# Optimization experiments

Measured on AMD Instinct MI355X. Metric: run time of the kernel, lower is better.

Reference implementation:

```python
import jax, jax.numpy as jnp
import numpy as np

N_NODES = 20000
N_EDGES = 320000
IN_CH = 256
HID_CH = 256   # 2 * out_channels
OUT_CH = 128


def gcn_conv(x, edge_index, W, b, n_nodes):
    """PyG GCNConv: linear transform, add self-loops, sym-normalized scatter-add."""
    x = x @ W  # [N, C_out]
    loop = jnp.arange(n_nodes, dtype=edge_index.dtype)
    row = jnp.concatenate([edge_index[0], loop])  # source nodes
    col = jnp.concatenate([edge_index[1], loop])  # destination nodes
    deg = jax.ops.segment_sum(jnp.ones_like(col, dtype=x.dtype), col,
                              num_segments=n_nodes)
    deg_inv_sqrt = jnp.where(deg > 0, jax.lax.rsqrt(deg), 0.0)
    norm = deg_inv_sqrt[row] * deg_inv_sqrt[col]  # [E+N]
    msg = x[row] * norm[:, None]                  # gather + scale
    out = jax.ops.segment_sum(msg, col, num_segments=n_nodes)  # scatter-add
    return out + b


def setup_inputs() -> dict:
    key = jax.random.key(0)
    k1, k2, k3, k4, k5 = jax.random.split(key, 5)
    doc_embeds = jax.random.normal(k1, (N_NODES, IN_CH), dtype=jnp.float32)
    edge_index = jax.random.randint(k2, (2, N_EDGES), 0, N_NODES, dtype=jnp.int64)
    # Glorot-style init for GCN weights, zero bias (PyG defaults)
    s1 = 1.0 / np.sqrt(IN_CH)
    s2 = 1.0 / np.sqrt(HID_CH)
    W1 = jax.random.uniform(k3, (IN_CH, HID_CH), jnp.float32, -s1, s1)
    b1 = jnp.zeros((HID_CH,), jnp.float32)
    W2 = jax.random.uniform(k4, (HID_CH, OUT_CH), jnp.float32, -s2, s2)
    b2 = jnp.zeros((OUT_CH,), jnp.float32)
    return {"doc_embeds": doc_embeds, "edge_index": edge_index,
            "W1": W1, "b1": b1, "W2": W2, "b2": b2}


def reference(doc_embeds, edge_index, W1, b1, W2, b2):
    n = doc_embeds.shape[0]
    x = jax.nn.relu(gcn_conv(doc_embeds, edge_index, W1, b1, n))
    x = gcn_conv(x, edge_index, W2, b2, n)
    return x
```

## Files before the change

kernel.cpp:

```cpp
#include <hip/hip_runtime.h>
#include <math.h>

#define N_NODES 20000
#define N_EDGES 320000
#define IN_CH   256
#define HID_CH  256
#define OUT_CH  128
#define CAP     64
#define GK      256

typedef __attribute__((ext_vector_type(8))) short short8;
typedef __attribute__((ext_vector_type(8))) unsigned short ushort8;
typedef __attribute__((ext_vector_type(4))) unsigned short ushort4v;
typedef __attribute__((ext_vector_type(2))) unsigned short ushort2v;
typedef __attribute__((ext_vector_type(4))) float floatx4;
typedef __attribute__((ext_vector_type(2))) float floatx2;
typedef __attribute__((ext_vector_type(2))) _Float16 half2v;

static __device__ __forceinline__ unsigned short f2bf(float f) {
    unsigned int u = __float_as_uint(f);
    u += 0x7FFFu + ((u >> 16) & 1u);
    return (unsigned short)(u >> 16);
}
static __device__ __forceinline__ float bf2f(unsigned short h) {
    return __uint_as_float(((unsigned int)h) << 16);
}

__global__ __launch_bounds__(256)
void prep_kernel(const float* __restrict__ W1, const float* __restrict__ W2,
                 const float* __restrict__ doc,
                 unsigned short* __restrict__ W1thi, unsigned short* __restrict__ W1tlo,
                 unsigned short* __restrict__ W2thi, unsigned short* __restrict__ W2tlo,
                 unsigned short* __restrict__ Ehi, unsigned short* __restrict__ Elo,
                 const int* __restrict__ row, const int* __restrict__ col,
                 int* __restrict__ deg, unsigned short* __restrict__ srcs) {
    const int g = blockIdx.x * blockDim.x + threadIdx.x;
    const int gsz = gridDim.x * blockDim.x;
    for (int t = g; t < (IN_CH * HID_CH) / 16; t += gsz) {
        int n = t >> 4;
        int kc = (t & 15) * 16;
        ushort8 h0, l0, h1, l1;
#pragma unroll
        for (int j = 0; j < 8; ++j) {
            float x = W1[(size_t)(kc + j) * HID_CH + n];
            h0[j] = f2bf(x); l0[j] = f2bf(x - bf2f(h0[j]));
            float y = W1[(size_t)(kc + 8 + j) * HID_CH + n];
            h1[j] = f2bf(y); l1[j] = f2bf(y - bf2f(h1[j]));
        }
        *(ushort8*)(W1thi + (size_t)n * IN_CH + kc)     = h0;
        *(ushort8*)(W1thi + (size_t)n * IN_CH + kc + 8) = h1;
        *(ushort8*)(W1tlo + (size_t)n * IN_CH + kc)     = l0;
        *(ushort8*)(W1tlo + (size_t)n * IN_CH + kc + 8) = l1;
    }
    for (int t = g; t < (HID_CH * OUT_CH) / 16; t += gsz) {
        int n = t >> 4;
        int kc = (t & 15) * 16;
        ushort8 h0, l0, h1, l1;
#pragma unroll
        for (int j = 0; j < 8; ++j) {
            float x = W2[(size_t)(kc + j) * OUT_CH + n];
            h0[j] = f2bf(x); l0[j] = f2bf(x - bf2f(h0[j]));
            float y = W2[(size_t)(kc + 8 + j) * OUT_CH + n];
            h1[j] = f2bf(y); l1[j] = f2bf(y - bf2f(h1[j]));
        }
        *(ushort8*)(W2thi + (size_t)n * HID_CH + kc)     = h0;
        *(ushort8*)(W2thi + (size_t)n * HID_CH + kc + 8) = h1;
        *(ushort8*)(W2tlo + (size_t)n * HID_CH + kc)     = l0;
        *(ushort8*)(W2tlo + (size_t)n * HID_CH + kc + 8) = l1;
    }
    for (int t = g; t < (N_NODES * IN_CH) / 16; t += gsz) {
        int node = t >> 4;
        int kc = (t & 15) * 16;
        const float* ap = doc + (size_t)node * IN_CH + kc;
        float4 f0 = *(const float4*)(ap);
        float4 f1 = *(const float4*)(ap + 4);
        float4 f2 = *(const float4*)(ap + 8);
        float4 f3 = *(const float4*)(ap + 12);
        float xs[16] = {f0.x, f0.y, f0.z, f0.w, f1.x, f1.y, f1.z, f1.w,
                        f2.x, f2.y, f2.z, f2.w, f3.x, f3.y, f3.z, f3.w};
        ushort8 h0, l0, h1, l1;
#pragma unroll
        for (int j = 0; j < 8; ++j) {
            h0[j] = f2bf(xs[j]);     l0[j] = f2bf(xs[j] - bf2f(h0[j]));
            h1[j] = f2bf(xs[8 + j]); l1[j] = f2bf(xs[8 + j] - bf2f(h1[j]));
        }
        *(ushort8*)(Ehi + (size_t)node * IN_CH + kc)     = h0;
        *(ushort8*)(Ehi + (size_t)node * IN_CH + kc + 8) = h1;
        *(ushort8*)(Elo + (size_t)node * IN_CH + kc)     = l0;
        *(ushort8*)(Elo + (size_t)node * IN_CH + kc + 8) = l1;
    }
    for (int i = g; i < N_EDGES; i += gsz) {
        int c = col[i];
        int r = row[i];
        int p = atomicAdd(&deg[c], 1);
        srcs[(size_t)c * CAP + p] = (unsigned short)r;
    }
}

template <int TN>
__global__ __launch_bounds__(256)
void gemm_mfma_kernel(const unsigned short* __restrict__ Ahi, const unsigned short* __restrict__ Alo,
                      const unsigned short* __restrict__ Bthi, const unsigned short* __restrict__ Btlo,
                      const int* __restrict__ deg, _Float16* __restrict__ C, int M, int N) {
    constexpr int NJ = TN / 32;
    __shared__ unsigned short As[2][64][36];
    __shared__ unsigned short Bs[2][TN][36];
    const int tid = threadIdx.x;
    const int m0 = blockIdx.y * 64;
    const int n0 = blockIdx.x * TN;
    const int lane = tid & 63;
    const int wave = tid >> 6;
    const int wr = (wave >> 1) * 32;
    const int wc = (wave & 1) * (TN / 2);
    const int lm = lane & 15;
    const int lk = (lane >> 4) * 8;

    floatx4 acc[2][NJ];
#pragma unroll
    for (int i = 0; i < 2; ++i)
#pragma unroll
        for (int j = 0; j < NJ; ++j) acc[i][j] = (floatx4){0.f, 0.f, 0.f, 0.f};

    const int ar  = tid >> 2;
    const int ako = (tid & 3) * 8;

    for (int k0 = 0; k0 < GK; k0 += 32) {
        {
            ushort8 vh = {}, vl = {};
            if (m0 + ar < M) {
                size_t ga = (size_t)(m0 + ar) * GK + k0 + ako;
                vh = *(const ushort8*)(Ahi + ga);
                vl = *(const ushort8*)(Alo + ga);
            }
            *(ushort8*)&As[0][ar][ako] = vh;
            *(ushort8*)&As[1][ar][ako] = vl;
        }
#pragma unroll
        for (int c = 0; c < TN / 64; ++c) {
            int ch = tid + c * 256;
            int r  = ch >> 2;
            int ko = (ch & 3) * 8;
            size_t gb = (size_t)(n0 + r) * GK + k0 + ko;
            *(ushort8*)&Bs[0][r][ko] = *(const ushort8*)(Bthi + gb);
            *(ushort8*)&Bs[1][r][ko] = *(const ushort8*)(Btlo + gb);
        }
        __syncthreads();

        short8 ah[2], al[2], bh[NJ], bl[NJ];
#pragma unroll
        for (int i = 0; i < 2; ++i) {
            ah[i] = *(const short8*)&As[0][wr + i * 16 + lm][lk];
            al[i] = *(const short8*)&As[1][wr + i * 16 + lm][lk];
        }
#pragma unroll
        for (int j = 0; j < NJ; ++j) {
            bh[j] = *(const short8*)&Bs[0][wc + j * 16 + lm][lk];
            bl[j] = *(const short8*)&Bs[1][wc + j * 16 + lm][lk];
        }
#pragma unroll
        for (int i = 0; i < 2; ++i)
#pragma unroll
            for (int j = 0; j < NJ; ++j) {
                acc[i][j] = __builtin_amdgcn_mfma_f32_16x16x32_bf16(ah[i], bh[j], acc[i][j], 0, 0, 0);
                acc[i][j] = __builtin_amdgcn_mfma_f32_16x16x32_bf16(ah[i], bl[j], acc[i][j], 0, 0, 0);
                acc[i][j] = __builtin_amdgcn_mfma_f32_16x16x32_bf16(al[i], bh[j], acc[i][j], 0, 0, 0);
            }
        __syncthreads();
    }

#pragma unroll
    for (int i = 0; i < 2; ++i) {
#pragma unroll
        for (int r = 0; r < 4; ++r) {
            int rowi = m0 + wr + i * 16 + (lane >> 4) * 4 + r;
            if (rowi < M) {
                float dr = 1.0f / sqrtf((float)(deg[rowi] + 1));
#pragma unroll
                for (int j = 0; j < NJ; ++j) {
                    C[(size_t)rowi * N + n0 + wc + j * 16 + lm] = (_Float16)(dr * acc[i][j][r]);
                }
            }
        }
    }
}

template <int C, int NSLICE, int MODE>
__global__ __launch_bounds__(256)
void gather_sliced_kernel(const _Float16* __restrict__ X, const int* __restrict__ deg,
                          const unsigned short* __restrict__ srcs,
                          const float* __restrict__ bias, float* __restrict__ outf,
                          unsigned short* __restrict__ outhi, unsigned short* __restrict__ outlo,
                          int n) {
    constexpr int SW = C / NSLICE;
    static_assert(SW == 32, "slice must be 32 channels");
    const int slice = blockIdx.x % NSLICE;
    const int ngrp  = blockIdx.x / NSLICE;
    const int wave = threadIdx.x >> 6;
    const int lane = threadIdx.x & 63;
    const int g  = lane >> 4;
    const int sl = lane & 15;
    const int node = ngrp * 16 + wave * 4 + g;
    if (node >= n) return;
    const int choff = slice * SW + sl * 2;
    const size_t beg = (size_t)node * CAP;
    const int cnt = deg[node];

    float a0 = 0.f, a1 = 0.f;
    int e = 0;
    for (; e + 4 <= cnt; e += 4) {
        ushort4v s4 = *(const ushort4v*)(srcs + beg + e);
        half2v v0 = *(const half2v*)(X + (size_t)s4.x * C + choff);
        half2v v1 = *(const half2v*)(X + (size_t)s4.y * C + choff);
        half2v v2 = *(const half2v*)(X + (size_t)s4.z * C + choff);
        half2v v3 = *(const half2v*)(X + (size_t)s4.w * C + choff);
        a0 += (float)v0.x + (float)v1.x + (float)v2.x + (float)v3.x;
        a1 += (float)v0.y + (float)v1.y + (float)v2.y + (float)v3.y;
    }
    for (; e < cnt; ++e) {
        int r = srcs[beg + e];
        half2v v = *(const half2v*)(X + (size_t)r * C + choff);
        a0 += (float)v.x; a1 += (float)v.y;
    }

    const float dc = 1.0f / sqrtf((float)(cnt + 1));
    half2v vsh = *(const half2v*)(X + (size_t)node * C + choff);
    float2 bb = *(const float2*)(bias + choff);

    float o0 = dc * (a0 + (float)vsh.x) + bb.x;
    float o1 = dc * (a1 + (float)vsh.y) + bb.y;

    if constexpr (MODE == 1) {
        float r0 = fmaxf(o0, 0.f), r1 = fmaxf(o1, 0.f);
        ushort2v hv, lv;
        hv.x = f2bf(r0); lv.x = f2bf(r0 - bf2f(hv.x));
        hv.y = f2bf(r1); lv.y = f2bf(r1 - bf2f(hv.y));
        *(ushort2v*)(outhi + (size_t)node * C + choff) = hv;
        *(ushort2v*)(outlo + (size_t)node * C + choff) = lv;
    } else {
        floatx2 o = {o0, o1};
        __builtin_nontemporal_store(o, (floatx2*)(outf + (size_t)node * C + choff));
    }
}

extern "C" void kernel_launch(void* const* d_in, const int* in_sizes, int n_in,
                              void* d_out, int out_size, void* d_ws, size_t ws_size,
                              hipStream_t stream) {
    const float* doc_embeds = (const float*)d_in[0];
    const int*   edge_index = (const int*)d_in[1];
    const float* W1 = (const float*)d_in[2];
    const float* b1 = (const float*)d_in[3];
    const float* W2 = (const float*)d_in[4];
    const float* b2 = (const float*)d_in[5];
    float* out = (float*)d_out;

    const int* row = edge_index;
    const int* col = edge_index + N_EDGES;

    char* ws = (char*)d_ws;
    auto au = [](size_t x) { return (x + 255) / 256 * 256; };

    _Float16* X1s = (_Float16*)ws;      ws += au((size_t)N_NODES * HID_CH * 2);
    unsigned short* Ehi  = (unsigned short*)ws; ws += au((size_t)N_NODES * IN_CH * 2);
    unsigned short* Elo  = (unsigned short*)ws; ws += au((size_t)N_NODES * IN_CH * 2);
    unsigned short* H1hi = (unsigned short*)ws; ws += au((size_t)N_NODES * HID_CH * 2);
    unsigned short* H1lo = (unsigned short*)ws; ws += au((size_t)N_NODES * HID_CH * 2);
    unsigned short* W1thi = (unsigned short*)ws; ws += au((size_t)IN_CH * HID_CH * 2);
    unsigned short* W1tlo = (unsigned short*)ws; ws += au((size_t)IN_CH * HID_CH * 2);
    unsigned short* W2thi = (unsigned short*)ws; ws += au((size_t)HID_CH * OUT_CH * 2);
    unsigned short* W2tlo = (unsigned short*)ws; ws += au((size_t)HID_CH * OUT_CH * 2);
    int*            deg   = (int*)ws;            ws += au((size_t)N_NODES * 4);
    unsigned short* srcs  = (unsigned short*)ws;

    hipMemsetAsync(deg, 0, (size_t)N_NODES * 4, stream);
    prep_kernel<<<(N_EDGES + 255) / 256, 256, 0, stream>>>(
        W1, W2, doc_embeds, W1thi, W1tlo, W2thi, W2tlo, Ehi, Elo, row, col, deg, srcs);

    {
        dim3 grid(HID_CH / 128, (N_NODES + 63) / 64);
        gemm_mfma_kernel<128><<<grid, 256, 0, stream>>>(
            Ehi, Elo, W1thi, W1tlo, deg, X1s, N_NODES, HID_CH);
    }
    gather_sliced_kernel<HID_CH, 8, 1><<<((N_NODES + 15) / 16) * 8, 256, 0, stream>>>(
        X1s, deg, srcs, b1, nullptr, H1hi, H1lo, N_NODES);

    {
        dim3 grid(OUT_CH / 64, (N_NODES + 63) / 64);
        gemm_mfma_kernel<64><<<grid, 256, 0, stream>>>(
            H1hi, H1lo, W2thi, W2tlo, deg, X1s, N_NODES, OUT_CH);
    }
    gather_sliced_kernel<OUT_CH, 4, 0><<<((N_NODES + 15) / 16) * 4, 256, 0, stream>>>(
        X1s, deg, srcs, b2, out, nullptr, nullptr, N_NODES);
}
```

Before: 181.9 us.

## Fuse fp32 split-bf16 conversion into GEMM1 and widen tiles and gather slices

The separate pass that split doc_embeds into hi/lo bf16 buffers is removed. GEMM1 now reads fp32 directly and does the split while staging to shared memory, which saves a full write and re-read of two 20000x256 bf16 arrays. Both GEMMs now cover the full N width in one block, so A is loaded once, and they declare a launch-bounds occupancy hint. The MFMA loop is reordered to load B fragments one at a time, and the gather kernels use 64-channel slices with 32 lanes per node. The trade-off is a larger accumulator per thread and therefore register pressure, plus fewer blocks in the GEMM grid.

Measured after the change: 176.3 us. 1.03x faster.

```diff
diff --git a/kernel.cpp b/kernel.cpp
--- a/kernel.cpp
+++ b/kernel.cpp
@@ -28,10 +28,8 @@
 
 __global__ __launch_bounds__(256)
 void prep_kernel(const float* __restrict__ W1, const float* __restrict__ W2,
-                 const float* __restrict__ doc,
                  unsigned short* __restrict__ W1thi, unsigned short* __restrict__ W1tlo,
                  unsigned short* __restrict__ W2thi, unsigned short* __restrict__ W2tlo,
-                 unsigned short* __restrict__ Ehi, unsigned short* __restrict__ Elo,
                  const int* __restrict__ row, const int* __restrict__ col,
                  int* __restrict__ deg, unsigned short* __restrict__ srcs) {
     const int g = blockIdx.x * blockDim.x + threadIdx.x;
@@ -68,27 +66,6 @@
         *(ushort8*)(W2tlo + (size_t)n * HID_CH + kc)     = l0;
         *(ushort8*)(W2tlo + (size_t)n * HID_CH + kc + 8) = l1;
     }
-    for (int t = g; t < (N_NODES * IN_CH) / 16; t += gsz) {
-        int node = t >> 4;
-        int kc = (t & 15) * 16;
-        const float* ap = doc + (size_t)node * IN_CH + kc;
-        float4 f0 = *(const float4*)(ap);
-        float4 f1 = *(const float4*)(ap + 4);
-        float4 f2 = *(const float4*)(ap + 8);
-        float4 f3 = *(const float4*)(ap + 12);
-        float xs[16] = {f0.x, f0.y, f0.z, f0.w, f1.x, f1.y, f1.z, f1.w,
-                        f2.x, f2.y, f2.z, f2.w, f3.x, f3.y, f3.z, f3.w};
-        ushort8 h0, l0, h1, l1;
-#pragma unroll
-        for (int j = 0; j < 8; ++j) {
-            h0[j] = f2bf(xs[j]);     l0[j] = f2bf(xs[j] - bf2f(h0[j]));
-            h1[j] = f2bf(xs[8 + j]); l1[j] = f2bf(xs[8 + j] - bf2f(h1[j]));
-        }
-        *(ushort8*)(Ehi + (size_t)node * IN_CH + kc)     = h0;
-        *(ushort8*)(Ehi + (size_t)node * IN_CH + kc + 8) = h1;
-        *(ushort8*)(Elo + (size_t)node * IN_CH + kc)     = l0;
-        *(ushort8*)(Elo + (size_t)node * IN_CH + kc + 8) = l1;
-    }
     for (int i = g; i < N_EDGES; i += gsz) {
         int c = col[i];
         int r = row[i];
@@ -97,9 +74,10 @@
     }
 }
 
-template <int TN>
-__global__ __launch_bounds__(256)
-void gemm_mfma_kernel(const unsigned short* __restrict__ Ahi, const unsigned short* __restrict__ Alo,
+template <int AMODE, int TN>
+__global__ __launch_bounds__(256, 2)
+void gemm_mfma_kernel(const float* __restrict__ Afp,
+                      const unsigned short* __restrict__ Ahi, const unsigned short* __restrict__ Alo,
                       const unsigned short* __restrict__ Bthi, const unsigned short* __restrict__ Btlo,
                       const int* __restrict__ deg, _Float16* __restrict__ C, int M, int N) {
     constexpr int NJ = TN / 32;
@@ -107,7 +85,6 @@
     __shared__ unsigned short Bs[2][TN][36];
     const int tid = threadIdx.x;
     const int m0 = blockIdx.y * 64;
-    const int n0 = blockIdx.x * TN;
     const int lane = tid & 63;
     const int wave = tid >> 6;
     const int wr = (wave >> 1) * 32;
@@ -128,9 +105,21 @@
         {
             ushort8 vh = {}, vl = {};
             if (m0 + ar < M) {
-                size_t ga = (size_t)(m0 + ar) * GK + k0 + ako;
-                vh = *(const ushort8*)(Ahi + ga);
-                vl = *(const ushort8*)(Alo + ga);
+                if (AMODE == 1) {
+                    const float* ap = Afp + (size_t)(m0 + ar) * GK + k0 + ako;
+                    float4 f0 = *(const float4*)ap;
+                    float4 f1 = *(const float4*)(ap + 4);
+                    float xs[8] = {f0.x, f0.y, f0.z, f0.w, f1.x, f1.y, f1.z, f1.w};
+#pragma unroll
+                    for (int j = 0; j < 8; ++j) {
+                        vh[j] = f2bf(xs[j]);
+                        vl[j] = f2bf(xs[j] - bf2f(vh[j]));
+                    }
+                } else {
+                    size_t ga = (size_t)(m0 + ar) * GK + k0 + ako;
+                    vh = *(const ushort8*)(Ahi + ga);
+                    vl = *(const ushort8*)(Alo + ga);
+                }
             }
             *(ushort8*)&As[0][ar][ako] = vh;
             *(ushort8*)&As[1][ar][ako] = vl;
@@ -140,13 +129,13 @@
             int ch = tid + c * 256;
             int r  = ch >> 2;
             int ko = (ch & 3) * 8;
-            size_t gb = (size_t)(n0 + r) * GK + k0 + ko;
+            size_t gb = (size_t)r * GK + k0 + ko;
             *(ushort8*)&Bs[0][r][ko] = *(const ushort8*)(Bthi + gb);
             *(ushort8*)&Bs[1][r][ko] = *(const ushort8*)(Btlo + gb);
         }
         __syncthreads();
 
-        short8 ah[2], al[2], bh[NJ], bl[NJ];
+        short8 ah[2], al[2];
 #pragma unroll
         for (int i = 0; i < 2; ++i) {
             ah[i] = *(const short8*)&As[0][wr + i * 16 + lm][lk];
@@ -154,17 +143,15 @@
         }
 #pragma unroll
         for (int j = 0; j < NJ; ++j) {
-            bh[j] = *(const short8*)&Bs[0][wc + j * 16 + lm][lk];
-            bl[j] = *(const short8*)&Bs[1][wc + j * 16 + lm][lk];
-        }
-#pragma unroll
-        for (int i = 0; i < 2; ++i)
-#pragma unroll
-            for (int j = 0; j < NJ; ++j) {
-                acc[i][j] = __builtin_amdgcn_mfma_f32_16x16x32_bf16(ah[i], bh[j], acc[i][j], 0, 0, 0);
-                acc[i][j] = __builtin_amdgcn_mfma_f32_16x16x32_bf16(ah[i], bl[j], acc[i][j], 0, 0, 0);
-                acc[i][j] = __builtin_amdgcn_mfma_f32_16x16x32_bf16(al[i], bh[j], acc[i][j], 0, 0, 0);
+            short8 bh = *(const short8*)&Bs[0][wc + j * 16 + lm][lk];
+            short8 bl = *(const short8*)&Bs[1][wc + j * 16 + lm][lk];
+#pragma unroll
+            for (int i = 0; i < 2; ++i) {
+                acc[i][j] = __builtin_amdgcn_mfma_f32_16x16x32_bf16(ah[i], bh, acc[i][j], 0, 0, 0);
+                acc[i][j] = __builtin_amdgcn_mfma_f32_16x16x32_bf16(ah[i], bl, acc[i][j], 0, 0, 0);
+                acc[i][j] = __builtin_amdgcn_mfma_f32_16x16x32_bf16(al[i], bh, acc[i][j], 0, 0, 0);
             }
+        }
         __syncthreads();
     }
 
@@ -177,7 +164,7 @@
                 float dr = 1.0f / sqrtf((float)(deg[rowi] + 1));
 #pragma unroll
                 for (int j = 0; j < NJ; ++j) {
-                    C[(size_t)rowi * N + n0 + wc + j * 16 + lm] = (_Float16)(dr * acc[i][j][r]);
+                    C[(size_t)rowi * N + wc + j * 16 + lm] = (_Float16)(dr * acc[i][j][r]);
                 }
             }
         }
@@ -192,14 +179,14 @@
                           unsigned short* __restrict__ outhi, unsigned short* __restrict__ outlo,
                           int n) {
     constexpr int SW = C / NSLICE;
-    static_assert(SW == 32, "slice must be 32 channels");
+    static_assert(SW == 64, "slice must be 64 channels");
     const int slice = blockIdx.x % NSLICE;
     const int ngrp  = blockIdx.x / NSLICE;
     const int wave = threadIdx.x >> 6;
     const int lane = threadIdx.x & 63;
-    const int g  = lane >> 4;
-    const int sl = lane & 15;
-    const int node = ngrp * 16 + wave * 4 + g;
+    const int gg = lane >> 5;
+    const int sl = lane & 31;
+    const int node = ngrp * 8 + wave * 2 + gg;
     if (node >= n) return;
     const int choff = slice * SW + sl * 2;
     const size_t beg = (size_t)node * CAP;
@@ -260,8 +247,6 @@
     auto au = [](size_t x) { return (x + 255) / 256 * 256; };
 
     _Float16* X1s = (_Float16*)ws;      ws += au((size_t)N_NODES * HID_CH * 2);
-    unsigned short* Ehi  = (unsigned short*)ws; ws += au((size_t)N_NODES * IN_CH * 2);
-    unsigned short* Elo  = (unsigned short*)ws; ws += au((size_t)N_NODES * IN_CH * 2);
     unsigned short* H1hi = (unsigned short*)ws; ws += au((size_t)N_NODES * HID_CH * 2);
     unsigned short* H1lo = (unsigned short*)ws; ws += au((size_t)N_NODES * HID_CH * 2);
     unsigned short* W1thi = (unsigned short*)ws; ws += au((size_t)IN_CH * HID_CH * 2);
@@ -273,21 +258,21 @@
 
     hipMemsetAsync(deg, 0, (size_t)N_NODES * 4, stream);
     prep_kernel<<<(N_EDGES + 255) / 256, 256, 0, stream>>>(
-        W1, W2, doc_embeds, W1thi, W1tlo, W2thi, W2tlo, Ehi, Elo, row, col, deg, srcs);
+        W1, W2, W1thi, W1tlo, W2thi, W2tlo, row, col, deg, srcs);
 
     {
-        dim3 grid(HID_CH / 128, (N_NODES + 63) / 64);
-        gemm_mfma_kernel<128><<<grid, 256, 0, stream>>>(
-            Ehi, Elo, W1thi, W1tlo, deg, X1s, N_NODES, HID_CH);
-    }
-    gather_sliced_kernel<HID_CH, 8, 1><<<((N_NODES + 15) / 16) * 8, 256, 0, stream>>>(
+        dim3 grid(1, (N_NODES + 63) / 64);
+        gemm_mfma_kernel<1, 256><<<grid, 256, 0, stream>>>(
+            doc_embeds, nullptr, nullptr, W1thi, W1tlo, deg, X1s, N_NODES, HID_CH);
+    }
+    gather_sliced_kernel<HID_CH, 4, 1><<<((N_NODES + 7) / 8) * 4, 256, 0, stream>>>(
         X1s, deg, srcs, b1, nullptr, H1hi, H1lo, N_NODES);
 
     {
-        dim3 grid(OUT_CH / 64, (N_NODES + 63) / 64);
-        gemm_mfma_kernel<64><<<grid, 256, 0, stream>>>(
-            H1hi, H1lo, W2thi, W2tlo, deg, X1s, N_NODES, OUT_CH);
-    }
-    gather_sliced_kernel<OUT_CH, 4, 0><<<((N_NODES + 15) / 16) * 4, 256, 0, stream>>>(
+        dim3 grid(1, (N_NODES + 63) / 64);
+        gemm_mfma_kernel<3, 128><<<grid, 256, 0, stream>>>(
+            nullptr, H1hi, H1lo, W2thi, W2tlo, deg, X1s, N_NODES, OUT_CH);
+    }
+    gather_sliced_kernel<OUT_CH, 2, 0><<<((N_NODES + 7) / 8) * 2, 256, 0, stream>>>(
         X1s, deg, srcs, b2, out, nullptr, nullptr, N_NODES);
 }
```
